# Performance work log

Measured on AMD Instinct MI355X. Metric: run time of the kernel, lower is better.

Reference implementation:

```python
import jax, jax.numpy as jnp
import numpy as np

EMBED = 512
INPUT = 512
NEGINF = -1000000.0


def setup_inputs() -> dict:
    key = jax.random.key(0)
    k1, k2, k3, k4, k5, k6, k7 = jax.random.split(key, 7)
    B, S = 8, 2048
    return {
        "Xin_q": jax.random.normal(k1, (B, S, INPUT), dtype=jnp.float32),
        "Xin_k": jax.random.normal(k2, (B, S, INPUT), dtype=jnp.float32),
        "Xin_v": jax.random.normal(k3, (B, S, INPUT), dtype=jnp.float32),
        "mask": jax.random.randint(k4, (B, S, S), 0, 2, dtype=jnp.int32),
        # Linear weights stored as (input, embed) so projection is x @ W
        "Wq": jax.random.normal(k5, (INPUT, EMBED), dtype=jnp.float32) / np.sqrt(INPUT),
        "Wk": jax.random.normal(k6, (INPUT, EMBED), dtype=jnp.float32) / np.sqrt(INPUT),
        "Wv": jax.random.normal(k7, (INPUT, EMBED), dtype=jnp.float32) / np.sqrt(INPUT),
    }


def reference(Xin_q, Xin_k, Xin_v, mask, Wq, Wk, Wv):
    scale = EMBED ** 0.25  # each of Q and K divided by d^(1/4) -> QK^T / sqrt(d)
    Xq = (Xin_q @ Wq) / scale          # [B,S,E]
    Xk = (Xin_k @ Wk) / scale          # [B,S,E]
    Xv = Xin_v @ Wv                    # [B,S,E]
    attn_w = jnp.einsum("bqe,bke->bqk", Xq, Xk)  # [B,S,S]
    attn_w = jnp.where(mask == 0, NEGINF, attn_w)
    attn_p = jax.nn.softmax(attn_w, axis=2)
    # post-softmax unnormalized mask-multiply (nonstandard)
    attn_p = attn_p * mask.astype(attn_p.dtype)
    z = jnp.einsum("bqk,bke->bqe", attn_p, Xv)   # [B,S,E]
    return (z, attn_p)
```

## Files before the change

### kernel.cpp

```cpp
#include <hip/hip_runtime.h>
#include <stdint.h>

typedef __attribute__((ext_vector_type(8))) short short8;
typedef __attribute__((ext_vector_type(4))) float f32x4;
typedef __attribute__((ext_vector_type(8))) unsigned short ushort8v;

#define NEGINF_F (-1000000.0f)

__device__ __forceinline__ unsigned short f2bf(float f) {
  union { float f; uint32_t u; } v; v.f = f;
  uint32_t r = (v.u + 0x7FFFu + ((v.u >> 16) & 1u)) >> 16;
  return (unsigned short)r;
}
__device__ __forceinline__ void gl_lds16(const void* g, void* l) {
  __builtin_amdgcn_global_load_lds(
      (const __attribute__((address_space(1))) void*)g,
      (__attribute__((address_space(3))) void*)l, 16, 0, 0);
}

template<bool A32, bool OUT32, bool MASKED>
__global__ __launch_bounds__(256, 2)
void gemm_nt(const void* __restrict__ Av, const unsigned short* __restrict__ B,
             void* __restrict__ Cv, const int* __restrict__ mask,
             int K, int lda, int ldb, int ldc,
             long sA, long sB, long sC, long sM, float scale)
{
  __shared__ __align__(16) unsigned char AsRaw[A32 ? 128*32*4 : 128*32*2];
  __shared__ unsigned short Bs[128 * 32];
  const int t = threadIdx.x;
  const int b = blockIdx.z;
  const float* Af = (const float*)Av + (long)b * sA;
  const unsigned short* Ah = (const unsigned short*)Av + (long)b * sA;
  const unsigned short* Bp = B + (long)b * sB;
  const int* mp = MASKED ? (mask + (long)b * sM) : nullptr;
  const int tm = blockIdx.x * 128;
  const int tn = blockIdx.y * 128;

  const int lane = t & 63, wave = t >> 6;
  const int wm = (wave & 1) * 64, wn = (wave >> 1) * 64;
  const int q = lane >> 4, mr = lane & 15;

  f32x4 acc[4][4];
#pragma unroll
  for (int i = 0; i < 4; i++)
#pragma unroll
    for (int j = 0; j < 4; j++) acc[i][j] = (f32x4){0.f, 0.f, 0.f, 0.f};

  const int r0a = t >> 2;
  const int c0a = (t & 3) * 8;

  for (int k0 = 0; k0 < K; k0 += 32) {
    __syncthreads();
    if (A32) {
      float* Asf = (float*)AsRaw;
#pragma unroll
      for (int rd = 0; rd < 4; rd++) {
        const int f = rd * 1024 + t * 4;
        const int row = f >> 5, col = f & 31;
        gl_lds16(Af + (long)(tm + row) * lda + k0 + col, Asf + f);
      }
    } else {
      unsigned short* Ash = (unsigned short*)AsRaw;
      const unsigned short* ga = Ah + (long)(tm + r0a) * lda + k0 + c0a;
      gl_lds16(ga, &Ash[(size_t)t * 8]);
      gl_lds16(ga + (long)64 * lda, &Ash[(size_t)(t + 256) * 8]);
    }
    {
      const unsigned short* gb = Bp + (long)(tn + r0a) * ldb + k0 + c0a;
      gl_lds16(gb, &Bs[(size_t)t * 8]);
      gl_lds16(gb + (long)64 * ldb, &Bs[(size_t)(t + 256) * 8]);
    }
    __syncthreads();

    short8 af[4], bfr[4];
#pragma unroll
    for (int i = 0; i < 4; i++) {
      if (A32) {
        const float* Asf = (const float*)AsRaw;
        const int base = (wm + i * 16 + mr) * 32 + q * 8;
        const f32x4 x0 = *(const f32x4*)&Asf[base];
        const f32x4 x1 = *(const f32x4*)&Asf[base + 4];
        short8 v;
        v[0] = (short)f2bf(x0[0]); v[1] = (short)f2bf(x0[1]);
        v[2] = (short)f2bf(x0[2]); v[3] = (short)f2bf(x0[3]);
        v[4] = (short)f2bf(x1[0]); v[5] = (short)f2bf(x1[1]);
        v[6] = (short)f2bf(x1[2]); v[7] = (short)f2bf(x1[3]);
        af[i] = v;
      } else {
        const unsigned short* Ash = (const unsigned short*)AsRaw;
        af[i] = *(const short8*)&Ash[(size_t)(wm + i * 16 + mr) * 32 + q * 8];
      }
      bfr[i] = *(const short8*)&Bs[(size_t)(wn + i * 16 + mr) * 32 + q * 8];
    }
#pragma unroll
    for (int i = 0; i < 4; i++)
#pragma unroll
      for (int j = 0; j < 4; j++)
        acc[i][j] = __builtin_amdgcn_mfma_f32_16x16x32_bf16(
            af[i], bfr[j], acc[i][j], 0, 0, 0);
  }

#pragma unroll
  for (int i = 0; i < 4; i++) {
#pragma unroll
    for (int j = 0; j < 4; j++) {
      const int row0 = tm + wm + i * 16 + q * 4;
      const int col  = tn + wn + j * 16 + mr;
      const f32x4 v = acc[i][j];
#pragma unroll
      for (int r = 0; r < 4; r++) {
        float x = v[r] * scale;
        if (MASKED) {
          const int mv = mp[(long)(row0 + r) * ldc + col];
          if (!mv) x = NEGINF_F;
        }
        if (OUT32) {
          ((float*)Cv + (long)b * sC)[(long)(row0 + r) * ldc + col] = x;
        } else {
          ((unsigned short*)Cv + (long)b * sC)[(long)(row0 + r) * ldc + col] = f2bf(x);
        }
      }
    }
  }
}

__global__ __launch_bounds__(256) void softmax_rows_f32(float* __restrict__ P)
{
  const int row = blockIdx.x;
  float* p = P + (size_t)row * 2048;
  const int t = threadIdx.x, lane = t & 63, wv = t >> 6;
  f32x4 a = *(const f32x4*)(p + t * 8);
  f32x4 c = *(const f32x4*)(p + t * 8 + 4);
  float x[8] = {a[0], a[1], a[2], a[3], c[0], c[1], c[2], c[3]};
  float mx = x[0];
#pragma unroll
  for (int j = 1; j < 8; j++) mx = fmaxf(mx, x[j]);
#pragma unroll
  for (int o = 32; o > 0; o >>= 1) mx = fmaxf(mx, __shfl_xor(mx, o));
  __shared__ float rm[4], rs[4];
  if (lane == 0) rm[wv] = mx;
  __syncthreads();
  mx = fmaxf(fmaxf(rm[0], rm[1]), fmaxf(rm[2], rm[3]));
  float e[8], s = 0.f;
#pragma unroll
  for (int j = 0; j < 8; j++) { e[j] = __expf(x[j] - mx); s += e[j]; }
#pragma unroll
  for (int o = 32; o > 0; o >>= 1) s += __shfl_xor(s, o);
  if (lane == 0) rs[wv] = s;
  __syncthreads();
  s = rs[0] + rs[1] + rs[2] + rs[3];
  const float linv = (mx < -1.0e5f) ? 0.f : 1.f / s;
  f32x4 o0 = {e[0] * linv, e[1] * linv, e[2] * linv, e[3] * linv};
  f32x4 o1 = {e[4] * linv, e[5] * linv, e[6] * linv, e[7] * linv};
  *(f32x4*)(p + t * 8) = o0;
  *(f32x4*)(p + t * 8 + 4) = o1;
}

__global__ __launch_bounds__(256) void cvt(
    const float* __restrict__ s, unsigned short* __restrict__ d)
{
  const size_t i = ((size_t)blockIdx.x * 256 + threadIdx.x) * 8;
  const float4 a = *(const float4*)(s + i);
  const float4 b = *(const float4*)(s + i + 4);
  ushort8v o;
  o[0] = f2bf(a.x); o[1] = f2bf(a.y); o[2] = f2bf(a.z); o[3] = f2bf(a.w);
  o[4] = f2bf(b.x); o[5] = f2bf(b.y); o[6] = f2bf(b.z); o[7] = f2bf(b.w);
  *(ushort8v*)(d + i) = o;
}

__global__ __launch_bounds__(256) void cvt_t_v(
    const float* __restrict__ src, unsigned short* __restrict__ dst)
{
  const int b = blockIdx.z;
  __shared__ float tile[32][33];
  const int s0 = blockIdx.x * 32, i0 = blockIdx.y * 32;
  const int tx = threadIdx.x & 31, ty = threadIdx.x >> 5;
#pragma unroll
  for (int r = 0; r < 4; r++) {
    const int srow = ty + r * 8;
    tile[srow][tx] = src[((size_t)b * 2048 + s0 + srow) * 512 + i0 + tx];
  }
  __syncthreads();
#pragma unroll
  for (int r = 0; r < 4; r++) {
    const int irow = ty + r * 8;
    dst[((size_t)b * 512 + i0 + irow) * 2048 + s0 + tx] = f2bf(tile[tx][irow]);
  }
}

__global__ __launch_bounds__(256) void transpose_w(
    const float* __restrict__ W0, const float* __restrict__ W1,
    const float* __restrict__ W2,
    unsigned short* __restrict__ T0, unsigned short* __restrict__ T1,
    unsigned short* __restrict__ T2)
{
  const float* W = blockIdx.z == 0 ? W0 : (blockIdx.z == 1 ? W1 : W2);
  unsigned short* T = blockIdx.z == 0 ? T0 : (blockIdx.z == 1 ? T1 : T2);
  __shared__ float tile[32][33];
  const int bx = blockIdx.x * 32, by = blockIdx.y * 32;
  const int tx = threadIdx.x & 31, ty = threadIdx.x >> 5;
#pragma unroll
  for (int i = 0; i < 4; i++) {
    const int r = ty + i * 8;
    tile[r][tx] = W[(size_t)(by + r) * 512 + bx + tx];
  }
  __syncthreads();
#pragma unroll
  for (int i = 0; i < 4; i++) {
    const int r = ty + i * 8;
    T[(size_t)(bx + r) * 512 + by + tx] = f2bf(tile[tx][r]);
  }
}

extern "C" void kernel_launch(void* const* d_in, const int* in_sizes, int n_in,
                              void* d_out, int out_size, void* d_ws, size_t ws_size,
                              hipStream_t stream) {
  const float* Xq = (const float*)d_in[0];
  const float* Xk = (const float*)d_in[1];
  const float* Xv = (const float*)d_in[2];
  const int*   mk = (const int*)d_in[3];
  const float* Wq = (const float*)d_in[4];
  const float* Wk = (const float*)d_in[5];
  const float* Wv = (const float*)d_in[6];

  float* z = (float*)d_out;
  float* P = z + (size_t)8 * 2048 * 512;

  unsigned short* w    = (unsigned short*)d_ws;
  unsigned short* Wtq  = w;
  unsigned short* Wtk  = w + 262144;
  unsigned short* Wtv  = w + 524288;
  unsigned short* buf1 = w + 786432;
  unsigned short* buf2 = buf1 + 8388608;
  unsigned short* Ks   = buf2 + 8388608;

  const float inv_scale = 0.21022410381342863f;

  transpose_w<<<dim3(16, 16, 3), 256, 0, stream>>>(Wq, Wk, Wv, Wtq, Wtk, Wtv);

  cvt<<<dim3(4096), 256, 0, stream>>>(Xq, buf1);
  gemm_nt<false, false, false><<<dim3(128, 4, 1), 256, 0, stream>>>(
      buf1, Wtq, buf2, nullptr, 512, 512, 512, 512, 0, 0, 0, 0, inv_scale);

  cvt<<<dim3(4096), 256, 0, stream>>>(Xk, buf1);
  gemm_nt<false, false, false><<<dim3(128, 4, 1), 256, 0, stream>>>(
      buf1, Wtk, Ks, nullptr, 512, 512, 512, 512, 0, 0, 0, 0, inv_scale);

  gemm_nt<false, true, true><<<dim3(16, 16, 8), 256, 0, stream>>>(
      buf2, Ks, P, mk, 512, 512, 512, 2048,
      1048576, 1048576, 4194304, 4194304, 1.0f);

  softmax_rows_f32<<<dim3(16384), 256, 0, stream>>>(P);

  cvt_t_v<<<dim3(64, 16, 8), 256, 0, stream>>>(Xv, buf1);
  gemm_nt<true, false, false><<<dim3(16, 4, 8), 256, 0, stream>>>(
      P, buf1, buf2, nullptr, 2048, 2048, 2048, 512,
      4194304, 1048576, 1048576, 0, 1.0f);
  gemm_nt<false, true, false><<<dim3(128, 4, 1), 256, 0, stream>>>(
      buf2, Wtv, z, nullptr, 512, 512, 512, 512, 0, 0, 0, 0, 1.0f);
}
```

Before: 539.6 us.

## Swizzle LDS tiles, stage fp32 epilogue through LDS, emit bf16 probabilities from softmax

Applies an XOR swizzle to the bf16 LDS tile layout to reduce bank conflicts on fragment reads. The fp32 output epilogue is restaged through shared memory so each thread writes and reads the mask with coalesced 16-byte vectors instead of scattered scalar accesses. Softmax also writes a bf16 copy of the probabilities, so the P@V GEMM reads half the bytes and skips the in-loop fp32-to-bf16 conversion. That bf16 path only runs when the workspace is large enough, and the epilogue adds extra syncs and LDS traffic.

```diff
diff --git a/kernel.cpp b/kernel.cpp
--- a/kernel.cpp
+++ b/kernel.cpp
@@ -3,6 +3,7 @@
 
 typedef __attribute__((ext_vector_type(8))) short short8;
 typedef __attribute__((ext_vector_type(4))) float f32x4;
+typedef __attribute__((ext_vector_type(4))) int i32x4;
 typedef __attribute__((ext_vector_type(8))) unsigned short ushort8v;
 
 #define NEGINF_F (-1000000.0f)
@@ -25,8 +26,13 @@
              int K, int lda, int ldb, int ldc,
              long sA, long sB, long sC, long sM, float scale)
 {
-  __shared__ __align__(16) unsigned char AsRaw[A32 ? 128*32*4 : 128*32*2];
-  __shared__ unsigned short Bs[128 * 32];
+  constexpr int ABYTES = A32 ? 128 * 32 * 4 : 128 * 32 * 2;
+  constexpr int BBYTES = 128 * 32 * 2;
+  constexpr int SMEM = (ABYTES + BBYTES) > 16384 ? (ABYTES + BBYTES) : 16384;
+  __shared__ __align__(16) unsigned char smem[SMEM];
+  unsigned char* AsRaw = smem;
+  unsigned short* Bs = (unsigned short*)(smem + ABYTES);
+
   const int t = threadIdx.x;
   const int b = blockIdx.z;
   const float* Af = (const float*)Av + (long)b * sA;
@@ -47,7 +53,8 @@
     for (int j = 0; j < 4; j++) acc[i][j] = (f32x4){0.f, 0.f, 0.f, 0.f};
 
   const int r0a = t >> 2;
-  const int c0a = (t & 3) * 8;
+  const int cswz = ((t & 3) ^ ((t >> 2) & 3)) * 8;
+  const int sw8 = (q ^ (mr & 3)) * 8;
 
   for (int k0 = 0; k0 < K; k0 += 32) {
     __syncthreads();
@@ -61,12 +68,12 @@
       }
     } else {
       unsigned short* Ash = (unsigned short*)AsRaw;
-      const unsigned short* ga = Ah + (long)(tm + r0a) * lda + k0 + c0a;
+      const unsigned short* ga = Ah + (long)(tm + r0a) * lda + k0 + cswz;
       gl_lds16(ga, &Ash[(size_t)t * 8]);
       gl_lds16(ga + (long)64 * lda, &Ash[(size_t)(t + 256) * 8]);
     }
     {
-      const unsigned short* gb = Bp + (long)(tn + r0a) * ldb + k0 + c0a;
+      const unsigned short* gb = Bp + (long)(tn + r0a) * ldb + k0 + cswz;
       gl_lds16(gb, &Bs[(size_t)t * 8]);
       gl_lds16(gb + (long)64 * ldb, &Bs[(size_t)(t + 256) * 8]);
     }
@@ -88,9 +95,9 @@
         af[i] = v;
       } else {
         const unsigned short* Ash = (const unsigned short*)AsRaw;
-        af[i] = *(const short8*)&Ash[(size_t)(wm + i * 16 + mr) * 32 + q * 8];
-      }
-      bfr[i] = *(const short8*)&Bs[(size_t)(wn + i * 16 + mr) * 32 + q * 8];
+        af[i] = *(const short8*)&Ash[(size_t)(wm + i * 16 + mr) * 32 + sw8];
+      }
+      bfr[i] = *(const short8*)&Bs[(size_t)(wn + i * 16 + mr) * 32 + sw8];
     }
 #pragma unroll
     for (int i = 0; i < 4; i++)
@@ -100,23 +107,55 @@
             af[i], bfr[j], acc[i][j], 0, 0, 0);
   }
 
-#pragma unroll
-  for (int i = 0; i < 4; i++) {
-#pragma unroll
-    for (int j = 0; j < 4; j++) {
-      const int row0 = tm + wm + i * 16 + q * 4;
-      const int col  = tn + wn + j * 16 + mr;
-      const f32x4 v = acc[i][j];
-#pragma unroll
-      for (int r = 0; r < 4; r++) {
-        float x = v[r] * scale;
+  if (OUT32) {
+    float* ep = (float*)smem;
+    float* co = (float*)Cv + (long)b * sC;
+    const int band = wm >> 2;
+    const int tr = t >> 3;
+    const int tcb = (t & 7) * 16;
+    const int growb = tm + (tr >> 4) * 64 + (tr & 15);
+#pragma unroll
+    for (int i = 0; i < 4; i++) {
+      __syncthreads();
+#pragma unroll
+      for (int j = 0; j < 4; j++) {
+        const int colb = wn + j * 16 + mr;
+#pragma unroll
+        for (int r = 0; r < 4; r++) {
+          const int lr = band + q * 4 + r;
+          ep[lr * 128 + ((colb + lr * 4) & 127)] = acc[i][j][r];
+        }
+      }
+      __syncthreads();
+      const int gr = growb + i * 16;
+      const long rbase = (long)gr * ldc;
+      const float* eprow = ep + tr * 128;
+      const int rot = tr * 4;
+#pragma unroll
+      for (int k = 0; k < 4; k++) {
+        const int lc = tcb + k * 4;
+        f32x4 x = *(const f32x4*)&eprow[(lc + rot) & 127];
+        x *= scale;
         if (MASKED) {
-          const int mv = mp[(long)(row0 + r) * ldc + col];
-          if (!mv) x = NEGINF_F;
+          const i32x4 mv = *(const i32x4*)&mp[rbase + tn + lc];
+#pragma unroll
+          for (int e = 0; e < 4; e++)
+            if (!mv[e]) x[e] = NEGINF_F;
         }
-        if (OUT32) {
-          ((float*)Cv + (long)b * sC)[(long)(row0 + r) * ldc + col] = x;
-        } else {
+        *(f32x4*)&co[rbase + tn + lc] = x;
+      }
+    }
+  } else {
+#pragma unroll
+    for (int i = 0; i < 4; i++) {
+#pragma unroll
+      for (int j = 0; j < 4; j++) {
+        const int row0 = tm + wm + i * 16 + q * 4;
+        const int col  = tn + wn + j * 16 + mr;
+        const f32x4 v = acc[i][j];
+#pragma unroll
+        for (int r = 0; r < 4; r++) {
+          float x = v[r] * scale;
           ((unsigned short*)Cv + (long)b * sC)[(long)(row0 + r) * ldc + col] = f2bf(x);
         }
       }
@@ -124,7 +163,8 @@
   }
 }
 
-__global__ __launch_bounds__(256) void softmax_rows_f32(float* __restrict__ P)
+__global__ __launch_bounds__(256) void softmax_rows_f32(
+    float* __restrict__ P, unsigned short* __restrict__ Pb)
 {
   const int row = blockIdx.x;
   float* p = P + (size_t)row * 2048;
@@ -154,6 +194,12 @@
   f32x4 o1 = {e[4] * linv, e[5] * linv, e[6] * linv, e[7] * linv};
   *(f32x4*)(p + t * 8) = o0;
   *(f32x4*)(p + t * 8 + 4) = o1;
+  if (Pb) {
+    ushort8v ob;
+    ob[0] = f2bf(o0[0]); ob[1] = f2bf(o0[1]); ob[2] = f2bf(o0[2]); ob[3] = f2bf(o0[3]);
+    ob[4] = f2bf(o1[0]); ob[5] = f2bf(o1[1]); ob[6] = f2bf(o1[2]); ob[7] = f2bf(o1[3]);
+    *(ushort8v*)(Pb + (size_t)row * 2048 + t * 8) = ob;
+  }
 }
 
 __global__ __launch_bounds__(256) void cvt(
@@ -233,6 +279,8 @@
   unsigned short* buf1 = w + 786432;
   unsigned short* buf2 = buf1 + 8388608;
   unsigned short* Ks   = buf2 + 8388608;
+  unsigned short* Pb   = Ks;
+  const bool use_pb = ws_size >= (size_t)102236160;
 
   const float inv_scale = 0.21022410381342863f;
 
@@ -250,12 +298,18 @@
       buf2, Ks, P, mk, 512, 512, 512, 2048,
       1048576, 1048576, 4194304, 4194304, 1.0f);
 
-  softmax_rows_f32<<<dim3(16384), 256, 0, stream>>>(P);
+  softmax_rows_f32<<<dim3(16384), 256, 0, stream>>>(P, use_pb ? Pb : nullptr);
 
   cvt_t_v<<<dim3(64, 16, 8), 256, 0, stream>>>(Xv, buf1);
-  gemm_nt<true, false, false><<<dim3(16, 4, 8), 256, 0, stream>>>(
-      P, buf1, buf2, nullptr, 2048, 2048, 2048, 512,
-      4194304, 1048576, 1048576, 0, 1.0f);
+  if (use_pb) {
+    gemm_nt<false, false, false><<<dim3(16, 4, 8), 256, 0, stream>>>(
+        Pb, buf1, buf2, nullptr, 2048, 2048, 2048, 512,
+        4194304, 1048576, 1048576, 0, 1.0f);
+  } else {
+    gemm_nt<true, false, false><<<dim3(16, 4, 8), 256, 0, stream>>>(
+        P, buf1, buf2, nullptr, 2048, 2048, 2048, 512,
+        4194304, 1048576, 1048576, 0, 1.0f);
+  }
   gemm_nt<false, true, false><<<dim3(128, 4, 1), 256, 0, stream>>>(
       buf2, Wtv, z, nullptr, 512, 512, 512, 512, 0, 0, 0, 0, 1.0f);
 }
```

After: 535.8 us. No clear change (-0.7%).
